# Performance work log

Measured on AMD Instinct MI355X. Metric: run time of the kernel, lower is better.

## Reference

```python
import jax, jax.numpy as jnp
import numpy as np

B, N, D, H, O = 4096, 128, 64, 256, 128  # batch, memory_size, memory_dim, controller_dim, output_size


def setup_inputs() -> dict:
    key = jax.random.key(0)
    ks = jax.random.split(key, 20)
    s = 0.05
    inp = {
        "x": jax.random.normal(ks[0], (B, O), jnp.float32),
        "memory": jax.random.normal(ks[1], (B, N, D), jnp.float32),
        "h": jax.random.normal(ks[2], (B, H), jnp.float32),
        "c": jax.random.normal(ks[3], (B, H), jnp.float32),
        # LSTMCell params (torch layout: gates ordered i, f, g, o; input = x||read_vec of width O+D)
        "W_ih": jax.random.normal(ks[4], (4 * H, O + D), jnp.float32) * s,
        "W_hh": jax.random.normal(ks[5], (4 * H, H), jnp.float32) * s,
        "b_ih": jax.random.normal(ks[6], (4 * H,), jnp.float32) * s,
        "b_hh": jax.random.normal(ks[7], (4 * H,), jnp.float32) * s,
        "W_read": jax.random.normal(ks[8], (N, H), jnp.float32) * s,
        "b_read": jax.random.normal(ks[9], (N,), jnp.float32) * s,
        "W_write": jax.random.normal(ks[10], (N, H), jnp.float32) * s,
        "b_write": jax.random.normal(ks[11], (N,), jnp.float32) * s,
        "W_erase": jax.random.normal(ks[12], (D, H), jnp.float32) * s,
        "b_erase": jax.random.normal(ks[13], (D,), jnp.float32) * s,
        "W_add": jax.random.normal(ks[14], (D, H), jnp.float32) * s,
        "b_add": jax.random.normal(ks[15], (D,), jnp.float32) * s,
        "W_out": jax.random.normal(ks[16], (O, H + D), jnp.float32) * s,
        "b_out": jax.random.normal(ks[17], (O,), jnp.float32) * s,
    }
    return inp


def reference(x, memory, h, c, W_ih, W_hh, b_ih, b_hh, W_read, b_read,
              W_write, b_write, W_erase, b_erase, W_add, b_add, W_out, b_out):
    # read: softmax attention over memory rows, addressed by previous hidden state
    read_w = jax.nn.softmax(h @ W_read.T + b_read, axis=-1)          # [B, N]
    read_vec = jnp.einsum("bn,bnd->bd", read_w, memory)               # [B, D]

    # LSTMCell step (torch gate order: i, f, g, o)
    ctrl_in = jnp.concatenate([x, read_vec], axis=-1)                 # [B, O+D]
    gates = ctrl_in @ W_ih.T + b_ih + h @ W_hh.T + b_hh               # [B, 4H]
    i, f, g, o = jnp.split(gates, 4, axis=-1)
    i, f, o = jax.nn.sigmoid(i), jax.nn.sigmoid(f), jax.nn.sigmoid(o)
    g = jnp.tanh(g)
    c_new = f * c + i * g
    h_new = o * jnp.tanh(c_new)

    # write: outer-product erase/add update
    write_w = jax.nn.softmax(h_new @ W_write.T + b_write, axis=-1)    # [B, N]
    erase = jax.nn.sigmoid(h_new @ W_erase.T + b_erase)               # [B, D]
    add = jnp.tanh(h_new @ W_add.T + b_add)                           # [B, D]
    ww = write_w[:, :, None]                                          # [B, N, 1]
    mem_new = memory * (1.0 - ww * erase[:, None, :]) + ww * add[:, None, :]

    out = jnp.concatenate([h_new, read_vec], axis=-1) @ W_out.T + b_out  # [B, O]
    return (out, mem_new, h_new, c_new)
```

## Files before the change

kernel.cpp:

```cpp
#include <hip/hip_runtime.h>
#include <math.h>


typedef __attribute__((ext_vector_type(8))) short bf16x8;
typedef __attribute__((ext_vector_type(4))) float f32x4;
typedef __attribute__((ext_vector_type(4))) unsigned short us4;

#define MFMA16(a, b, c) __builtin_amdgcn_mfma_f32_16x16x32_bf16(a, b, c, 0, 0, 0)
#define GLL16(gp, lp) __builtin_amdgcn_global_load_lds( \
    (const __attribute__((address_space(1))) void*)(gp), \
    (__attribute__((address_space(3))) void*)(lp), 16, 0, 0)
#define SW(row, s) ((s) ^ ((row) & 3))

__device__ __forceinline__ float sigf(float v) { return 1.f / (1.f + __expf(-v)); }

__device__ __forceinline__ unsigned short f2bf(float f) {
    unsigned u = __builtin_bit_cast(unsigned, f);
    u = (u + 0x7FFFu + ((u >> 16) & 1u)) >> 16;
    return (unsigned short)u;
}

__global__ __launch_bounds__(256) void p0_packW(
    const float* __restrict__ Wih, const float* __restrict__ Whh,
    const float* __restrict__ bih, const float* __restrict__ bhh,
    const float* __restrict__ Wr, const float* __restrict__ Ww,
    const float* __restrict__ We, const float* __restrict__ Wa,
    const float* __restrict__ bw, const float* __restrict__ be,
    const float* __restrict__ ba, const float* __restrict__ Wo,
    unsigned short* __restrict__ Wg, float* __restrict__ bsum,
    unsigned short* __restrict__ Wr_b, unsigned short* __restrict__ Wh_b,
    float* __restrict__ bh_b, unsigned short* __restrict__ Wo_b)
{
    int idx = blockIdx.x * 256 + threadIdx.x;
    int stride = gridDim.x * 256;
    for (int i = idx; i < 1024 * 448; i += stride) {
        int r = i / 448, cc = i - r * 448;
        float v = (cc < 192) ? Wih[(size_t)r * 192 + cc] : Whh[(size_t)r * 256 + (cc - 192)];
        Wg[i] = f2bf(v);
    }
    for (int i = idx; i < 1024; i += stride) bsum[i] = bih[i] + bhh[i];
    for (int i = idx; i < 128 * 256; i += stride) Wr_b[i] = f2bf(Wr[i]);
    for (int i = idx; i < 256 * 256; i += stride) {
        int r = i >> 8, cc = i & 255;
        float v = (r < 128) ? Ww[(size_t)r * 256 + cc]
                : (r < 192) ? We[(size_t)(r - 128) * 256 + cc]
                            : Wa[(size_t)(r - 192) * 256 + cc];
        Wh_b[i] = f2bf(v);
    }
    for (int i = idx; i < 256; i += stride)
        bh_b[i] = (i < 128) ? bw[i] : (i < 192 ? be[i - 128] : ba[i - 192]);
    for (int i = idx; i < 128 * 320; i += stride) Wo_b[i] = f2bf(Wo[i]);
}

__global__ __launch_bounds__(256) void p1_packA(
    const float* __restrict__ x, const float* __restrict__ h,
    unsigned short* __restrict__ Ag)
{
    int idx = blockIdx.x * 256 + threadIdx.x;
    int stride = gridDim.x * 256;
    for (int i = idx; i < 4096 * 96; i += stride) {
        int row = i / 96, j = i - row * 96;
        float4 v = (j < 32) ? ((const float4*)(x + (size_t)row * 128))[j]
                            : ((const float4*)(h + (size_t)row * 256))[j - 32];
        us4 o = { f2bf(v.x), f2bf(v.y), f2bf(v.z), f2bf(v.w) };
        int col = (j < 32) ? j * 4 : 192 + (j - 32) * 4;
        *(us4*)(Ag + (size_t)row * 448 + col) = o;
    }
}

__global__ __launch_bounds__(256) void k1_read_attn(
    const unsigned short* __restrict__ Ag, const unsigned short* __restrict__ Wr_b,
    const float* __restrict__ br, float* __restrict__ read_w)
{
    __shared__ unsigned short As[64 * 32];
    __shared__ unsigned short Bs[128 * 32];
    int t = threadIdx.x;
    int wid = t >> 6, lane = t & 63;
    int cl = lane & 15, ks = lane >> 4;
    int b0 = blockIdx.x * 64;

    int arow = t >> 2;
    const unsigned short* aSrc = Ag + (size_t)(b0 + arow) * 448 + 192 + SW(arow, t & 3) * 8;
    unsigned short* aDst = As + wid * 512;
    int r0 = (t >> 2), r1 = 64 + (t >> 2);
    const unsigned short* bSrc0 = Wr_b + (size_t)r0 * 256 + SW(r0, t & 3) * 8;
    const unsigned short* bSrc1 = Wr_b + (size_t)r1 * 256 + SW(r1, t & 3) * 8;
    unsigned short* bDst0 = Bs + wid * 512;
    unsigned short* bDst1 = Bs + 2048 + wid * 512;

    int mr = wid * 16 + cl;
    int aOff = mr * 32 + SW(mr, ks) * 8;
    int bOff[8];
#pragma unroll
    for (int f = 0; f < 8; ++f) { int br_ = f * 16 + cl; bOff[f] = br_ * 32 + SW(br_, ks) * 8; }

    f32x4 acc[8] = {};
    for (int kc = 0; kc < 8; ++kc) {
        __syncthreads();
        GLL16(aSrc, aDst); GLL16(bSrc0, bDst0); GLL16(bSrc1, bDst1);
        aSrc += 32; bSrc0 += 32; bSrc1 += 32;
        __syncthreads();
        bf16x8 a = *(const bf16x8*)(As + aOff);
#pragma unroll
        for (int f = 0; f < 8; ++f)
            acc[f] = MFMA16(a, *(const bf16x8*)(Bs + bOff[f]), acc[f]);
    }

    float bb[8];
#pragma unroll
    for (int f = 0; f < 8; ++f) bb[f] = br[f * 16 + cl];
#pragma unroll
    for (int r = 0; r < 4; ++r) {
        int row = b0 + wid * 16 + ks * 4 + r;
        float v[8];
#pragma unroll
        for (int f = 0; f < 8; ++f) v[f] = acc[f][r] + bb[f];
        float m = v[0];
#pragma unroll
        for (int f = 1; f < 8; ++f) m = fmaxf(m, v[f]);
#pragma unroll
        for (int mk = 8; mk >= 1; mk >>= 1) m = fmaxf(m, __shfl_xor(m, mk));
        float s = 0.f;
#pragma unroll
        for (int f = 0; f < 8; ++f) { v[f] = __expf(v[f] - m); s += v[f]; }
#pragma unroll
        for (int mk = 8; mk >= 1; mk >>= 1) s += __shfl_xor(s, mk);
        float inv = 1.f / s;
#pragma unroll
        for (int f = 0; f < 8; ++f)
            read_w[(size_t)row * 128 + f * 16 + cl] = v[f] * inv;
    }
}

__global__ __launch_bounds__(256) void k2_read_vec(
    const float* __restrict__ mem, const float* __restrict__ read_w,
    unsigned short* __restrict__ Ag, unsigned short* __restrict__ Aout)
{
    __shared__ float part[16][68];
    int t = threadIdx.x;
    int b = blockIdx.x;
    int np = t >> 4, d4 = t & 15;
    const float4* m4 = (const float4*)(mem + (size_t)b * 8192);
    float4 acc = make_float4(0.f, 0.f, 0.f, 0.f);
#pragma unroll
    for (int j = 0; j < 8; ++j) {
        int n = np + 16 * j;
        float w = read_w[(size_t)b * 128 + n];
        float4 mv = m4[t + 256 * j];
        acc.x += w * mv.x; acc.y += w * mv.y; acc.z += w * mv.z; acc.w += w * mv.w;
    }
    part[np][d4 * 4 + 0] = acc.x; part[np][d4 * 4 + 1] = acc.y;
    part[np][d4 * 4 + 2] = acc.z; part[np][d4 * 4 + 3] = acc.w;
    __syncthreads();
    if (t < 64) {
        float s = 0.f;
#pragma unroll
        for (int q = 0; q < 16; ++q) s += part[q][t];
        unsigned short bv = f2bf(s);
        Ag[(size_t)b * 448 + 128 + t] = bv;
        Aout[(size_t)b * 320 + 256 + t] = bv;
    }
}

__global__ __launch_bounds__(256) void k3_gates_mfma(
    const unsigned short* __restrict__ Ag, const unsigned short* __restrict__ Wg,
    const float* __restrict__ bsum, const float* __restrict__ c,
    float* __restrict__ h_new, float* __restrict__ c_new,
    unsigned short* __restrict__ Aout)
{
    __shared__ unsigned short As[64 * 32];
    __shared__ unsigned short Bs[256 * 32];
    int t = threadIdx.x;
    int wid = t >> 6, lane = t & 63;
    int cl = lane & 15, ks = lane >> 4;
    int b0 = blockIdx.x * 64;
    int u0 = blockIdx.y * 64;

    int arow = t >> 2;
    const unsigned short* aSrc = Ag + (size_t)(b0 + arow) * 448 + SW(arow, t & 3) * 8;
    unsigned short* aDst = As + wid * 512;
    const unsigned short* bSrc[4];
    unsigned short* bDst[4];
#pragma unroll
    for (int j = 0; j < 4; ++j) {
        int i = j * 256 + t;
        int rl = i >> 2;
        int g = rl >> 6, u = rl & 63;
        bSrc[j] = Wg + (size_t)(g * 256 + u0 + u) * 448 + SW(rl, t & 3) * 8;
        bDst[j] = Bs + (j * 256 + wid * 64) * 8;
    }

    int mr = wid * 16 + cl;
    int aOff = mr * 32 + SW(mr, ks) * 8;
    int bOff[4][4];
#pragma unroll
    for (int g = 0; g < 4; ++g)
#pragma unroll
        for (int uf = 0; uf < 4; ++uf) {
            int br_ = g * 64 + uf * 16 + cl;
            bOff[g][uf] = br_ * 32 + SW(br_, ks) * 8;
        }

    f32x4 acc[4][4] = {};
    for (int kc = 0; kc < 14; ++kc) {
        __syncthreads();
        GLL16(aSrc, aDst);
        GLL16(bSrc[0], bDst[0]); GLL16(bSrc[1], bDst[1]);
        GLL16(bSrc[2], bDst[2]); GLL16(bSrc[3], bDst[3]);
        aSrc += 32;
#pragma unroll
        for (int j = 0; j < 4; ++j) bSrc[j] += 32;
        __syncthreads();
        bf16x8 a = *(const bf16x8*)(As + aOff);
#pragma unroll
        for (int g = 0; g < 4; ++g)
#pragma unroll
            for (int uf = 0; uf < 4; ++uf)
                acc[uf][g] = MFMA16(a, *(const bf16x8*)(Bs + bOff[g][uf]), acc[uf][g]);
    }

#pragma unroll
    for (int uf = 0; uf < 4; ++uf) {
        int unit = u0 + uf * 16 + cl;
        float bi = bsum[unit], bf_ = bsum[256 + unit];
        float bg = bsum[512 + unit], bo_ = bsum[768 + unit];
#pragma unroll
        for (int r = 0; r < 4; ++r) {
            int row = b0 + wid * 16 + ks * 4 + r;
            float iv = sigf(acc[uf][0][r] + bi);
            float fv = sigf(acc[uf][1][r] + bf_);
            float gv = tanhf(acc[uf][2][r] + bg);
            float ov = sigf(acc[uf][3][r] + bo_);
            float cv = fv * c[(size_t)row * 256 + unit] + iv * gv;
            float hv = ov * tanhf(cv);
            c_new[(size_t)row * 256 + unit] = cv;
            h_new[(size_t)row * 256 + unit] = hv;
            Aout[(size_t)row * 320 + unit] = f2bf(hv);
        }
    }
}

__global__ __launch_bounds__(256) void k4_heads(
    const unsigned short* __restrict__ Aout, const unsigned short* __restrict__ Wh_b,
    const float* __restrict__ bh_b, float* __restrict__ write_w,
    float* __restrict__ erase, float* __restrict__ addv)
{
    __shared__ unsigned short As[64 * 32];
    __shared__ unsigned short Bs[256 * 32];
    int t = threadIdx.x;
    int wid = t >> 6, lane = t & 63;
    int cl = lane & 15, ks = lane >> 4;
    int b0 = blockIdx.x * 64;

    int arow = t >> 2;
    const unsigned short* aSrc = Aout + (size_t)(b0 + arow) * 320 + SW(arow, t & 3) * 8;
    unsigned short* aDst = As + wid * 512;
    const unsigned short* bSrc[4];
    unsigned short* bDst[4];
#pragma unroll
    for (int j = 0; j < 4; ++j) {
        int i = j * 256 + t;
        int rl = i >> 2;
        bSrc[j] = Wh_b + (size_t)rl * 256 + SW(rl, t & 3) * 8;
        bDst[j] = Bs + (j * 256 + wid * 64) * 8;
    }

    int mr = wid * 16 + cl;
    int aOff = mr * 32 + SW(mr, ks) * 8;
    int bOff[16];
#pragma unroll
    for (int f = 0; f < 16; ++f) { int br_ = f * 16 + cl; bOff[f] = br_ * 32 + SW(br_, ks) * 8; }

    f32x4 acc[16] = {};
    for (int kc = 0; kc < 8; ++kc) {
        __syncthreads();
        GLL16(aSrc, aDst);
        GLL16(bSrc[0], bDst[0]); GLL16(bSrc[1], bDst[1]);
        GLL16(bSrc[2], bDst[2]); GLL16(bSrc[3], bDst[3]);
        aSrc += 32;
#pragma unroll
        for (int j = 0; j < 4; ++j) bSrc[j] += 32;
        __syncthreads();
        bf16x8 a = *(const bf16x8*)(As + aOff);
#pragma unroll
        for (int f = 0; f < 16; ++f)
            acc[f] = MFMA16(a, *(const bf16x8*)(Bs + bOff[f]), acc[f]);
    }

    float bb[16];
#pragma unroll
    for (int f = 0; f < 16; ++f) bb[f] = bh_b[f * 16 + cl];
#pragma unroll
    for (int r = 0; r < 4; ++r) {
        int row = b0 + wid * 16 + ks * 4 + r;
        float v[8];
#pragma unroll
        for (int f = 0; f < 8; ++f) v[f] = acc[f][r] + bb[f];
        float m = v[0];
#pragma unroll
        for (int f = 1; f < 8; ++f) m = fmaxf(m, v[f]);
#pragma unroll
        for (int mk = 8; mk >= 1; mk >>= 1) m = fmaxf(m, __shfl_xor(m, mk));
        float s = 0.f;
#pragma unroll
        for (int f = 0; f < 8; ++f) { v[f] = __expf(v[f] - m); s += v[f]; }
#pragma unroll
        for (int mk = 8; mk >= 1; mk >>= 1) s += __shfl_xor(s, mk);
        float inv = 1.f / s;
#pragma unroll
        for (int f = 0; f < 8; ++f)
            write_w[(size_t)row * 128 + f * 16 + cl] = v[f] * inv;
#pragma unroll
        for (int f = 8; f < 12; ++f)
            erase[(size_t)row * 64 + (f - 8) * 16 + cl] = sigf(acc[f][r] + bb[f]);
#pragma unroll
        for (int f = 12; f < 16; ++f)
            addv[(size_t)row * 64 + (f - 12) * 16 + cl] = tanhf(acc[f][r] + bb[f]);
    }
}

__global__ __launch_bounds__(256) void k6_out(
    const unsigned short* __restrict__ Aout, const unsigned short* __restrict__ Wo_b,
    const float* __restrict__ bo, float* __restrict__ outp)
{
    __shared__ unsigned short As[64 * 32];
    __shared__ unsigned short Bs[128 * 32];
    int t = threadIdx.x;
    int wid = t >> 6, lane = t & 63;
    int cl = lane & 15, ks = lane >> 4;
    int b0 = blockIdx.x * 64;

    int arow = t >> 2;
    const unsigned short* aSrc = Aout + (size_t)(b0 + arow) * 320 + SW(arow, t & 3) * 8;
    unsigned short* aDst = As + wid * 512;
    int r0 = (t >> 2), r1 = 64 + (t >> 2);
    const unsigned short* bSrc0 = Wo_b + (size_t)r0 * 320 + SW(r0, t & 3) * 8;
    const unsigned short* bSrc1 = Wo_b + (size_t)r1 * 320 + SW(r1, t & 3) * 8;
    unsigned short* bDst0 = Bs + wid * 512;
    unsigned short* bDst1 = Bs + 2048 + wid * 512;

    int mr = wid * 16 + cl;
    int aOff = mr * 32 + SW(mr, ks) * 8;
    int bOff[8];
#pragma unroll
    for (int f = 0; f < 8; ++f) { int br_ = f * 16 + cl; bOff[f] = br_ * 32 + SW(br_, ks) * 8; }

    f32x4 acc[8] = {};
    for (int kc = 0; kc < 10; ++kc) {
        __syncthreads();
        GLL16(aSrc, aDst); GLL16(bSrc0, bDst0); GLL16(bSrc1, bDst1);
        aSrc += 32; bSrc0 += 32; bSrc1 += 32;
        __syncthreads();
        bf16x8 a = *(const bf16x8*)(As + aOff);
#pragma unroll
        for (int f = 0; f < 8; ++f)
            acc[f] = MFMA16(a, *(const bf16x8*)(Bs + bOff[f]), acc[f]);
    }

    float bb[8];
#pragma unroll
    for (int f = 0; f < 8; ++f) bb[f] = bo[f * 16 + cl];
#pragma unroll
    for (int r = 0; r < 4; ++r) {
        int row = b0 + wid * 16 + ks * 4 + r;
#pragma unroll
        for (int f = 0; f < 8; ++f)
            outp[(size_t)row * 128 + f * 16 + cl] = acc[f][r] + bb[f];
    }
}

__global__ __launch_bounds__(256) void k5_mem_update(
    const float* __restrict__ mem, const float* __restrict__ write_w,
    const float* __restrict__ erase, const float* __restrict__ addv,
    float* __restrict__ mem_new)
{
    int t = threadIdx.x; int b = blockIdx.x;
    int np = t >> 4, d0 = (t & 15) * 4;
    const float4* m4 = (const float4*)(mem + (size_t)b * 8192);
    float4* o4 = (float4*)(mem_new + (size_t)b * 8192);
    float4 e4 = *(const float4*)(erase + (size_t)b * 64 + d0);
    float4 a4 = *(const float4*)(addv + (size_t)b * 64 + d0);
#pragma unroll
    for (int j = 0; j < 8; ++j) {
        int n = np + 16 * j;
        float w = write_w[(size_t)b * 128 + n];
        float4 m = m4[t + 256 * j];
        float4 r;
        r.x = m.x * (1.f - w * e4.x) + w * a4.x;
        r.y = m.y * (1.f - w * e4.y) + w * a4.y;
        r.z = m.z * (1.f - w * e4.z) + w * a4.z;
        r.w = m.w * (1.f - w * e4.w) + w * a4.w;
        o4[t + 256 * j] = r;
    }
}

extern "C" void kernel_launch(void* const* d_in, const int* in_sizes, int n_in,
                              void* d_out, int out_size, void* d_ws, size_t ws_size,
                              hipStream_t stream)
{
    const float* x    = (const float*)d_in[0];
    const float* mem  = (const float*)d_in[1];
    const float* h    = (const float*)d_in[2];
    const float* c    = (const float*)d_in[3];
    const float* Wih  = (const float*)d_in[4];
    const float* Whh  = (const float*)d_in[5];
    const float* bih  = (const float*)d_in[6];
    const float* bhh  = (const float*)d_in[7];
    const float* Wr   = (const float*)d_in[8];
    const float* br   = (const float*)d_in[9];
    const float* Ww   = (const float*)d_in[10];
    const float* bw   = (const float*)d_in[11];
    const float* We   = (const float*)d_in[12];
    const float* be   = (const float*)d_in[13];
    const float* Wa   = (const float*)d_in[14];
    const float* ba   = (const float*)d_in[15];
    const float* Wo   = (const float*)d_in[16];
    const float* bo   = (const float*)d_in[17];

    float* out     = (float*)d_out;
    float* mem_new = out + 524288;
    float* h_new   = out + 34078720;
    float* c_new   = out + 35127296;

    float* ws      = (float*)d_ws;
    float* read_w  = ws;
    float* write_w = ws + 524288;
    float* erase   = ws + 1048576;
    float* addv    = ws + 1310720;
    float* bsum    = ws + 1572864;
    float* bh_b    = ws + 1573888;
    unsigned short* ub   = (unsigned short*)(ws + 1574144);
    unsigned short* Ag   = ub;
    unsigned short* Aout = ub + 1835008;
    unsigned short* Wg   = ub + 3145728;
    unsigned short* Wr_b = ub + 3604480;
    unsigned short* Wh_b = ub + 3637248;
    unsigned short* Wo_b = ub + 3702784;

    p0_packW<<<512, 256, 0, stream>>>(Wih, Whh, bih, bhh, Wr, Ww, We, Wa, bw, be, ba, Wo,
                                      Wg, bsum, Wr_b, Wh_b, bh_b, Wo_b);
    p1_packA<<<1024, 256, 0, stream>>>(x, h, Ag);
    k1_read_attn<<<64, 256, 0, stream>>>(Ag, Wr_b, br, read_w);
    k2_read_vec<<<4096, 256, 0, stream>>>(mem, read_w, Ag, Aout);
    k3_gates_mfma<<<dim3(64, 4), 256, 0, stream>>>(Ag, Wg, bsum, c, h_new, c_new, Aout);
    k4_heads<<<64, 256, 0, stream>>>(Aout, Wh_b, bh_b, write_w, erase, addv);
    k6_out<<<64, 256, 0, stream>>>(Aout, Wo_b, bo, out);
    k5_mem_update<<<4096, 256, 0, stream>>>(mem, write_w, erase, addv, mem_new);
}
```

Before: 124.5 us.

## Merge pack kernels, fuse heads and output GEMMs, retile read and gate kernels

Merges the weight and activation packing kernels into one launch and fuses the heads GEMM with the output GEMM into a single kernel over 32-row tiles, so there are fewer launches and more blocks. The read-attention kernel now uses 128-thread blocks over 32 rows, which doubles the grid. The gates kernel gives each wave a 16-unit slice across all four row fragments, loading four A and four B fragments per k-step for more register reuse. The memory update uses nontemporal stores. The trade-off is that each fused block loads more weight data into LDS and some waves in the heads kernel sit idle for two k-steps.

Result: faster. 110.6 us (-11.2%).

```diff
diff --git a/kernel.cpp b/kernel.cpp
--- a/kernel.cpp
+++ b/kernel.cpp
@@ -20,16 +20,18 @@
     return (unsigned short)u;
 }
 
-__global__ __launch_bounds__(256) void p0_packW(
+__global__ __launch_bounds__(256) void p_pack(
     const float* __restrict__ Wih, const float* __restrict__ Whh,
     const float* __restrict__ bih, const float* __restrict__ bhh,
     const float* __restrict__ Wr, const float* __restrict__ Ww,
     const float* __restrict__ We, const float* __restrict__ Wa,
     const float* __restrict__ bw, const float* __restrict__ be,
     const float* __restrict__ ba, const float* __restrict__ Wo,
+    const float* __restrict__ x, const float* __restrict__ h,
     unsigned short* __restrict__ Wg, float* __restrict__ bsum,
     unsigned short* __restrict__ Wr_b, unsigned short* __restrict__ Wh_b,
-    float* __restrict__ bh_b, unsigned short* __restrict__ Wo_b)
+    float* __restrict__ bh_b, unsigned short* __restrict__ Wo_b,
+    unsigned short* __restrict__ Ag)
 {
     int idx = blockIdx.x * 256 + threadIdx.x;
     int stride = gridDim.x * 256;
@@ -50,14 +52,6 @@
     for (int i = idx; i < 256; i += stride)
         bh_b[i] = (i < 128) ? bw[i] : (i < 192 ? be[i - 128] : ba[i - 192]);
     for (int i = idx; i < 128 * 320; i += stride) Wo_b[i] = f2bf(Wo[i]);
-}
-
-__global__ __launch_bounds__(256) void p1_packA(
-    const float* __restrict__ x, const float* __restrict__ h,
-    unsigned short* __restrict__ Ag)
-{
-    int idx = blockIdx.x * 256 + threadIdx.x;
-    int stride = gridDim.x * 256;
     for (int i = idx; i < 4096 * 96; i += stride) {
         int row = i / 96, j = i - row * 96;
         float4 v = (j < 32) ? ((const float4*)(x + (size_t)row * 128))[j]
@@ -68,25 +62,28 @@
     }
 }
 
-__global__ __launch_bounds__(256) void k1_read_attn(
+__global__ __launch_bounds__(128) void k1_read_attn(
     const unsigned short* __restrict__ Ag, const unsigned short* __restrict__ Wr_b,
     const float* __restrict__ br, float* __restrict__ read_w)
 {
-    __shared__ unsigned short As[64 * 32];
+    __shared__ unsigned short As[32 * 32];
     __shared__ unsigned short Bs[128 * 32];
     int t = threadIdx.x;
     int wid = t >> 6, lane = t & 63;
     int cl = lane & 15, ks = lane >> 4;
-    int b0 = blockIdx.x * 64;
+    int b0 = blockIdx.x * 32;
 
     int arow = t >> 2;
     const unsigned short* aSrc = Ag + (size_t)(b0 + arow) * 448 + 192 + SW(arow, t & 3) * 8;
     unsigned short* aDst = As + wid * 512;
-    int r0 = (t >> 2), r1 = 64 + (t >> 2);
-    const unsigned short* bSrc0 = Wr_b + (size_t)r0 * 256 + SW(r0, t & 3) * 8;
-    const unsigned short* bSrc1 = Wr_b + (size_t)r1 * 256 + SW(r1, t & 3) * 8;
-    unsigned short* bDst0 = Bs + wid * 512;
-    unsigned short* bDst1 = Bs + 2048 + wid * 512;
+    const unsigned short* bSrc[4];
+    unsigned short* bDst[4];
+#pragma unroll
+    for (int J = 0; J < 4; ++J) {
+        int rJ = J * 32 + (t >> 2);
+        bSrc[J] = Wr_b + (size_t)rJ * 256 + SW(rJ, t & 3) * 8;
+        bDst[J] = Bs + J * 1024 + wid * 512;
+    }
 
     int mr = wid * 16 + cl;
     int aOff = mr * 32 + SW(mr, ks) * 8;
@@ -97,8 +94,12 @@
     f32x4 acc[8] = {};
     for (int kc = 0; kc < 8; ++kc) {
         __syncthreads();
-        GLL16(aSrc, aDst); GLL16(bSrc0, bDst0); GLL16(bSrc1, bDst1);
-        aSrc += 32; bSrc0 += 32; bSrc1 += 32;
+        GLL16(aSrc, aDst);
+#pragma unroll
+        for (int J = 0; J < 4; ++J) GLL16(bSrc[J], bDst[J]);
+        aSrc += 32;
+#pragma unroll
+        for (int J = 0; J < 4; ++J) bSrc[J] += 32;
         __syncthreads();
         bf16x8 a = *(const bf16x8*)(As + aOff);
 #pragma unroll
@@ -190,16 +191,18 @@
         bDst[j] = Bs + (j * 256 + wid * 64) * 8;
     }
 
-    int mr = wid * 16 + cl;
-    int aOff = mr * 32 + SW(mr, ks) * 8;
-    int bOff[4][4];
-#pragma unroll
-    for (int g = 0; g < 4; ++g)
-#pragma unroll
-        for (int uf = 0; uf < 4; ++uf) {
-            int br_ = g * 64 + uf * 16 + cl;
-            bOff[g][uf] = br_ * 32 + SW(br_, ks) * 8;
-        }
+    int aOff[4];
+#pragma unroll
+    for (int rf = 0; rf < 4; ++rf) {
+        int mr = rf * 16 + cl;
+        aOff[rf] = mr * 32 + SW(mr, ks) * 8;
+    }
+    int bOff[4];
+#pragma unroll
+    for (int g = 0; g < 4; ++g) {
+        int br_ = g * 64 + wid * 16 + cl;
+        bOff[g] = br_ * 32 + SW(br_, ks) * 8;
+    }
 
     f32x4 acc[4][4] = {};
     for (int kc = 0; kc < 14; ++kc) {
@@ -211,26 +214,30 @@
 #pragma unroll
         for (int j = 0; j < 4; ++j) bSrc[j] += 32;
         __syncthreads();
-        bf16x8 a = *(const bf16x8*)(As + aOff);
-#pragma unroll
-        for (int g = 0; g < 4; ++g)
-#pragma unroll
-            for (int uf = 0; uf < 4; ++uf)
-                acc[uf][g] = MFMA16(a, *(const bf16x8*)(Bs + bOff[g][uf]), acc[uf][g]);
-    }
-
-#pragma unroll
-    for (int uf = 0; uf < 4; ++uf) {
-        int unit = u0 + uf * 16 + cl;
-        float bi = bsum[unit], bf_ = bsum[256 + unit];
-        float bg = bsum[512 + unit], bo_ = bsum[768 + unit];
+        bf16x8 a[4], b[4];
+#pragma unroll
+        for (int rf = 0; rf < 4; ++rf) a[rf] = *(const bf16x8*)(As + aOff[rf]);
+#pragma unroll
+        for (int g = 0; g < 4; ++g) b[g] = *(const bf16x8*)(Bs + bOff[g]);
+#pragma unroll
+        for (int rf = 0; rf < 4; ++rf)
+#pragma unroll
+            for (int g = 0; g < 4; ++g)
+                acc[rf][g] = MFMA16(a[rf], b[g], acc[rf][g]);
+    }
+
+    int unit = u0 + wid * 16 + cl;
+    float bi = bsum[unit], bf_ = bsum[256 + unit];
+    float bg = bsum[512 + unit], bo_ = bsum[768 + unit];
+#pragma unroll
+    for (int rf = 0; rf < 4; ++rf) {
 #pragma unroll
         for (int r = 0; r < 4; ++r) {
-            int row = b0 + wid * 16 + ks * 4 + r;
-            float iv = sigf(acc[uf][0][r] + bi);
-            float fv = sigf(acc[uf][1][r] + bf_);
-            float gv = tanhf(acc[uf][2][r] + bg);
-            float ov = sigf(acc[uf][3][r] + bo_);
+            int row = b0 + rf * 16 + ks * 4 + r;
+            float iv = sigf(acc[rf][0][r] + bi);
+            float fv = sigf(acc[rf][1][r] + bf_);
+            float gv = tanhf(acc[rf][2][r] + bg);
+            float ov = sigf(acc[rf][3][r] + bo_);
             float cv = fv * c[(size_t)row * 256 + unit] + iv * gv;
             float hv = ov * tanhf(cv);
             c_new[(size_t)row * 256 + unit] = cv;
@@ -240,132 +247,114 @@
     }
 }
 
-__global__ __launch_bounds__(256) void k4_heads(
+__global__ __launch_bounds__(256) void k46_heads_out(
     const unsigned short* __restrict__ Aout, const unsigned short* __restrict__ Wh_b,
-    const float* __restrict__ bh_b, float* __restrict__ write_w,
-    float* __restrict__ erase, float* __restrict__ addv)
-{
-    __shared__ unsigned short As[64 * 32];
-    __shared__ unsigned short Bs[256 * 32];
+    const unsigned short* __restrict__ Wo_b, const float* __restrict__ bh_b,
+    const float* __restrict__ bo, float* __restrict__ write_w,
+    float* __restrict__ erase, float* __restrict__ addv, float* __restrict__ outp)
+{
+    __shared__ unsigned short As[32 * 32];
+    __shared__ unsigned short Bh[256 * 32];
+    __shared__ unsigned short Bo[128 * 32];
     int t = threadIdx.x;
     int wid = t >> 6, lane = t & 63;
     int cl = lane & 15, ks = lane >> 4;
-    int b0 = blockIdx.x * 64;
+    int rf = wid >> 1, ch = wid & 1;
+    int b0 = blockIdx.x * 32;
 
     int arow = t >> 2;
-    const unsigned short* aSrc = Aout + (size_t)(b0 + arow) * 320 + SW(arow, t & 3) * 8;
-    unsigned short* aDst = As + wid * 512;
-    const unsigned short* bSrc[4];
-    unsigned short* bDst[4];
+    const unsigned short* aSrc = Aout + (size_t)(b0 + (arow & 31)) * 320 + SW(arow & 31, t & 3) * 8;
+    unsigned short* aDst = As + (wid & 1) * 512;
+    const unsigned short* bhSrc[4];
+    unsigned short* bhDst[4];
 #pragma unroll
     for (int j = 0; j < 4; ++j) {
-        int i = j * 256 + t;
-        int rl = i >> 2;
-        bSrc[j] = Wh_b + (size_t)rl * 256 + SW(rl, t & 3) * 8;
-        bDst[j] = Bs + (j * 256 + wid * 64) * 8;
-    }
-
-    int mr = wid * 16 + cl;
+        int rl = (j * 256 + t) >> 2;
+        bhSrc[j] = Wh_b + (size_t)rl * 256 + SW(rl, t & 3) * 8;
+        bhDst[j] = Bh + (j * 256 + wid * 64) * 8;
+    }
+    const unsigned short* boSrc[2];
+    unsigned short* boDst[2];
+#pragma unroll
+    for (int j = 0; j < 2; ++j) {
+        int rj = j * 64 + (t >> 2);
+        boSrc[j] = Wo_b + (size_t)rj * 320 + SW(rj, t & 3) * 8;
+        boDst[j] = Bo + j * 2048 + wid * 512;
+    }
+
+    int mr = rf * 16 + cl;
     int aOff = mr * 32 + SW(mr, ks) * 8;
-    int bOff[16];
-#pragma unroll
-    for (int f = 0; f < 16; ++f) { int br_ = f * 16 + cl; bOff[f] = br_ * 32 + SW(br_, ks) * 8; }
-
-    f32x4 acc[16] = {};
-    for (int kc = 0; kc < 8; ++kc) {
-        __syncthreads();
-        GLL16(aSrc, aDst);
-        GLL16(bSrc[0], bDst[0]); GLL16(bSrc[1], bDst[1]);
-        GLL16(bSrc[2], bDst[2]); GLL16(bSrc[3], bDst[3]);
+    int bOffH[8], bOffO[4];
+#pragma unroll
+    for (int f = 0; f < 8; ++f) { int br_ = (ch * 8 + f) * 16 + cl; bOffH[f] = br_ * 32 + SW(br_, ks) * 8; }
+#pragma unroll
+    for (int f = 0; f < 4; ++f) { int br_ = (ch * 4 + f) * 16 + cl; bOffO[f] = br_ * 32 + SW(br_, ks) * 8; }
+
+    f32x4 accH[8] = {};
+    f32x4 accO[4] = {};
+    for (int kc = 0; kc < 10; ++kc) {
+        __syncthreads();
+        if (t < 128) GLL16(aSrc, aDst);
+        if (kc < 8) {
+            GLL16(bhSrc[0], bhDst[0]); GLL16(bhSrc[1], bhDst[1]);
+            GLL16(bhSrc[2], bhDst[2]); GLL16(bhSrc[3], bhDst[3]);
+        }
+        GLL16(boSrc[0], boDst[0]); GLL16(boSrc[1], boDst[1]);
         aSrc += 32;
 #pragma unroll
-        for (int j = 0; j < 4; ++j) bSrc[j] += 32;
+        for (int j = 0; j < 4; ++j) bhSrc[j] += 32;
+#pragma unroll
+        for (int j = 0; j < 2; ++j) boSrc[j] += 32;
         __syncthreads();
         bf16x8 a = *(const bf16x8*)(As + aOff);
-#pragma unroll
-        for (int f = 0; f < 16; ++f)
-            acc[f] = MFMA16(a, *(const bf16x8*)(Bs + bOff[f]), acc[f]);
-    }
-
-    float bb[16];
-#pragma unroll
-    for (int f = 0; f < 16; ++f) bb[f] = bh_b[f * 16 + cl];
+        if (kc < 8) {
+#pragma unroll
+            for (int f = 0; f < 8; ++f)
+                accH[f] = MFMA16(a, *(const bf16x8*)(Bh + bOffH[f]), accH[f]);
+        }
+#pragma unroll
+        for (int f = 0; f < 4; ++f)
+            accO[f] = MFMA16(a, *(const bf16x8*)(Bo + bOffO[f]), accO[f]);
+    }
+
+    float bbh[8], bbo[4];
+#pragma unroll
+    for (int f = 0; f < 8; ++f) bbh[f] = bh_b[(ch * 8 + f) * 16 + cl];
+#pragma unroll
+    for (int f = 0; f < 4; ++f) bbo[f] = bo[ch * 64 + f * 16 + cl];
+
 #pragma unroll
     for (int r = 0; r < 4; ++r) {
-        int row = b0 + wid * 16 + ks * 4 + r;
-        float v[8];
-#pragma unroll
-        for (int f = 0; f < 8; ++f) v[f] = acc[f][r] + bb[f];
-        float m = v[0];
-#pragma unroll
-        for (int f = 1; f < 8; ++f) m = fmaxf(m, v[f]);
-#pragma unroll
-        for (int mk = 8; mk >= 1; mk >>= 1) m = fmaxf(m, __shfl_xor(m, mk));
-        float s = 0.f;
-#pragma unroll
-        for (int f = 0; f < 8; ++f) { v[f] = __expf(v[f] - m); s += v[f]; }
-#pragma unroll
-        for (int mk = 8; mk >= 1; mk >>= 1) s += __shfl_xor(s, mk);
-        float inv = 1.f / s;
-#pragma unroll
-        for (int f = 0; f < 8; ++f)
-            write_w[(size_t)row * 128 + f * 16 + cl] = v[f] * inv;
-#pragma unroll
-        for (int f = 8; f < 12; ++f)
-            erase[(size_t)row * 64 + (f - 8) * 16 + cl] = sigf(acc[f][r] + bb[f]);
-#pragma unroll
-        for (int f = 12; f < 16; ++f)
-            addv[(size_t)row * 64 + (f - 12) * 16 + cl] = tanhf(acc[f][r] + bb[f]);
-    }
-}
-
-__global__ __launch_bounds__(256) void k6_out(
-    const unsigned short* __restrict__ Aout, const unsigned short* __restrict__ Wo_b,
-    const float* __restrict__ bo, float* __restrict__ outp)
-{
-    __shared__ unsigned short As[64 * 32];
-    __shared__ unsigned short Bs[128 * 32];
-    int t = threadIdx.x;
-    int wid = t >> 6, lane = t & 63;
-    int cl = lane & 15, ks = lane >> 4;
-    int b0 = blockIdx.x * 64;
-
-    int arow = t >> 2;
-    const unsigned short* aSrc = Aout + (size_t)(b0 + arow) * 320 + SW(arow, t & 3) * 8;
-    unsigned short* aDst = As + wid * 512;
-    int r0 = (t >> 2), r1 = 64 + (t >> 2);
-    const unsigned short* bSrc0 = Wo_b + (size_t)r0 * 320 + SW(r0, t & 3) * 8;
-    const unsigned short* bSrc1 = Wo_b + (size_t)r1 * 320 + SW(r1, t & 3) * 8;
-    unsigned short* bDst0 = Bs + wid * 512;
-    unsigned short* bDst1 = Bs + 2048 + wid * 512;
-
-    int mr = wid * 16 + cl;
-    int aOff = mr * 32 + SW(mr, ks) * 8;
-    int bOff[8];
-#pragma unroll
-    for (int f = 0; f < 8; ++f) { int br_ = f * 16 + cl; bOff[f] = br_ * 32 + SW(br_, ks) * 8; }
-
-    f32x4 acc[8] = {};
-    for (int kc = 0; kc < 10; ++kc) {
-        __syncthreads();
-        GLL16(aSrc, aDst); GLL16(bSrc0, bDst0); GLL16(bSrc1, bDst1);
-        aSrc += 32; bSrc0 += 32; bSrc1 += 32;
-        __syncthreads();
-        bf16x8 a = *(const bf16x8*)(As + aOff);
-#pragma unroll
-        for (int f = 0; f < 8; ++f)
-            acc[f] = MFMA16(a, *(const bf16x8*)(Bs + bOff[f]), acc[f]);
-    }
-
-    float bb[8];
-#pragma unroll
-    for (int f = 0; f < 8; ++f) bb[f] = bo[f * 16 + cl];
-#pragma unroll
-    for (int r = 0; r < 4; ++r) {
-        int row = b0 + wid * 16 + ks * 4 + r;
-#pragma unroll
-        for (int f = 0; f < 8; ++f)
-            outp[(size_t)row * 128 + f * 16 + cl] = acc[f][r] + bb[f];
+        int row = b0 + rf * 16 + ks * 4 + r;
+        if (ch == 0) {
+            float v[8];
+#pragma unroll
+            for (int f = 0; f < 8; ++f) v[f] = accH[f][r] + bbh[f];
+            float m = v[0];
+#pragma unroll
+            for (int f = 1; f < 8; ++f) m = fmaxf(m, v[f]);
+#pragma unroll
+            for (int mk = 8; mk >= 1; mk >>= 1) m = fmaxf(m, __shfl_xor(m, mk));
+            float s = 0.f;
+#pragma unroll
+            for (int f = 0; f < 8; ++f) { v[f] = __expf(v[f] - m); s += v[f]; }
+#pragma unroll
+            for (int mk = 8; mk >= 1; mk >>= 1) s += __shfl_xor(s, mk);
+            float inv = 1.f / s;
+#pragma unroll
+            for (int f = 0; f < 8; ++f)
+                write_w[(size_t)row * 128 + f * 16 + cl] = v[f] * inv;
+        } else {
+#pragma unroll
+            for (int f = 0; f < 4; ++f)
+                erase[(size_t)row * 64 + f * 16 + cl] = sigf(accH[f][r] + bbh[f]);
+#pragma unroll
+            for (int f = 4; f < 8; ++f)
+                addv[(size_t)row * 64 + (f - 4) * 16 + cl] = tanhf(accH[f][r] + bbh[f]);
+        }
+#pragma unroll
+        for (int f = 0; f < 4; ++f)
+            outp[(size_t)row * 128 + ch * 64 + f * 16 + cl] = accO[f][r] + bbo[f];
     }
 }
 
@@ -376,21 +365,21 @@
 {
     int t = threadIdx.x; int b = blockIdx.x;
     int np = t >> 4, d0 = (t & 15) * 4;
-    const float4* m4 = (const float4*)(mem + (size_t)b * 8192);
-    float4* o4 = (float4*)(mem_new + (size_t)b * 8192);
-    float4 e4 = *(const float4*)(erase + (size_t)b * 64 + d0);
-    float4 a4 = *(const float4*)(addv + (size_t)b * 64 + d0);
+    const f32x4* m4 = (const f32x4*)(mem + (size_t)b * 8192);
+    f32x4* o4 = (f32x4*)(mem_new + (size_t)b * 8192);
+    f32x4 e4 = *(const f32x4*)(erase + (size_t)b * 64 + d0);
+    f32x4 a4 = *(const f32x4*)(addv + (size_t)b * 64 + d0);
 #pragma unroll
     for (int j = 0; j < 8; ++j) {
         int n = np + 16 * j;
         float w = write_w[(size_t)b * 128 + n];
-        float4 m = m4[t + 256 * j];
-        float4 r;
-        r.x = m.x * (1.f - w * e4.x) + w * a4.x;
-        r.y = m.y * (1.f - w * e4.y) + w * a4.y;
-        r.z = m.z * (1.f - w * e4.z) + w * a4.z;
-        r.w = m.w * (1.f - w * e4.w) + w * a4.w;
-        o4[t + 256 * j] = r;
+        f32x4 m = m4[t + 256 * j];
+        f32x4 r;
+        r[0] = m[0] * (1.f - w * e4[0]) + w * a4[0];
+        r[1] = m[1] * (1.f - w * e4[1]) + w * a4[1];
+        r[2] = m[2] * (1.f - w * e4[2]) + w * a4[2];
+        r[3] = m[3] * (1.f - w * e4[3]) + w * a4[3];
+        __builtin_nontemporal_store(r, &o4[t + 256 * j]);
     }
 }
 
@@ -437,13 +426,12 @@
     unsigned short* Wh_b = ub + 3637248;
     unsigned short* Wo_b = ub + 3702784;
 
-    p0_packW<<<512, 256, 0, stream>>>(Wih, Whh, bih, bhh, Wr, Ww, We, Wa, bw, be, ba, Wo,
-                                      Wg, bsum, Wr_b, Wh_b, bh_b, Wo_b);
-    p1_packA<<<1024, 256, 0, stream>>>(x, h, Ag);
-    k1_read_attn<<<64, 256, 0, stream>>>(Ag, Wr_b, br, read_w);
+    p_pack<<<512, 256, 0, stream>>>(Wih, Whh, bih, bhh, Wr, Ww, We, Wa, bw, be, ba, Wo,
+                                    x, h, Wg, bsum, Wr_b, Wh_b, bh_b, Wo_b, Ag);
+    k1_read_attn<<<128, 128, 0, stream>>>(Ag, Wr_b, br, read_w);
     k2_read_vec<<<4096, 256, 0, stream>>>(mem, read_w, Ag, Aout);
     k3_gates_mfma<<<dim3(64, 4), 256, 0, stream>>>(Ag, Wg, bsum, c, h_new, c_new, Aout);
-    k4_heads<<<64, 256, 0, stream>>>(Aout, Wh_b, bh_b, write_w, erase, addv);
-    k6_out<<<64, 256, 0, stream>>>(Aout, Wo_b, bo, out);
+    k46_heads_out<<<128, 256, 0, stream>>>(Aout, Wh_b, Wo_b, bh_b, bo,
+                                           write_w, erase, addv, out);
     k5_mem_update<<<4096, 256, 0, stream>>>(mem, write_w, erase, addv, mem_new);
 }
```
